# Performance work log

Measured on AMD Instinct MI355X. Metric: run time of the kernel, lower is better.

## Reference

```python
import jax, jax.numpy as jnp
import numpy as np

BS, NUM_RELS, NUM_NODES, EMB = 8, 16, 512, 256


def setup_inputs() -> dict:
    key = jax.random.key(0)
    k1, k2, k3, k4 = jax.random.split(key, 4)
    features = jax.random.normal(k1, (BS, NUM_NODES, EMB), dtype=jnp.float32)
    adjacency = jax.random.uniform(k2, (BS, NUM_RELS, NUM_NODES, NUM_NODES), dtype=jnp.float32)
    # xavier_uniform bounds
    bound = float(np.sqrt(6.0 / (EMB + EMB)))
    W_r = jax.random.uniform(k3, (NUM_RELS, EMB, EMB), minval=-bound, maxval=bound, dtype=jnp.float32)
    W_0 = jax.random.uniform(k4, (EMB, EMB), minval=-bound, maxval=bound, dtype=jnp.float32)
    return {"features": features, "adjacency": adjacency, "W_r": W_r, "W_0": W_0}


def reference(features, adjacency, W_r, W_0):
    # msg[b,r,n,d] = sum_m adjacency[b,r,n,m] * features[b,m,d]
    msg = jnp.einsum('brnm,bmd->brnd', adjacency, features)
    # per-relation projection then sum over relations: [b,n,h]
    features_1 = jnp.einsum('brnd,rdh->bnh', msg, W_r)
    features_2 = jnp.einsum('bnd,dh->bnh', features, W_0)
    return jax.nn.relu(features_1 + features_2)
```

## Files before the change

kernel.cpp:

```cpp
#include <hip/hip_runtime.h>
#include <hip/hip_bf16.h>

#define BS   8
#define NREL 16
#define NN   512
#define EMB  256

typedef float f32x4 __attribute__((ext_vector_type(4)));
typedef short s16x8 __attribute__((ext_vector_type(8)));

__device__ __forceinline__ unsigned short f2bf_bits(float f) {
    union { float f; unsigned u; } v; v.f = f;
    unsigned r = (v.u + 0x7FFFu + ((v.u >> 16) & 1u)) >> 16;
    return (unsigned short)r;
}

__device__ __forceinline__ float bf2f(unsigned short u) {
    union { unsigned u; float f; } v; v.u = ((unsigned)u) << 16;
    return v.f;
}

__device__ __forceinline__ unsigned short f2bf_hw(float f) {
    union { __hip_bfloat16 h; unsigned short u; } v;
    v.h = __float2bfloat16(f);
    return v.u;
}

__global__ __launch_bounds__(256) void k0_prep(
        const float* __restrict__ Wr, const float* __restrict__ W0,
        const float* __restrict__ F,
        unsigned short* __restrict__ wT, unsigned short* __restrict__ Fbf) {
    int bid = blockIdx.x;
    if (bid < 1088) {
        __shared__ float tile[32][33];
        int rel = bid / 64;
        int t   = bid % 64;
        int d0  = (t & 7) * 32;
        int h0  = (t >> 3) * 32;
        int tx  = threadIdx.x & 31;
        int ty  = threadIdx.x >> 5;
        const float* src = (rel < NREL) ? (Wr + rel * (EMB * EMB)) : W0;
#pragma unroll
        for (int k = 0; k < 4; ++k) {
            int d = d0 + ty + k * 8;
            tile[ty + k * 8][tx] = src[d * EMB + h0 + tx];
        }
        __syncthreads();
#pragma unroll
        for (int k = 0; k < 4; ++k) {
            int h = h0 + ty + k * 8;
            wT[(rel * EMB + h) * EMB + d0 + tx] = f2bf_bits(tile[tx][ty + k * 8]);
        }
    } else {
        long i = ((long)(bid - 1088) * 256 + threadIdx.x) * 8;
        f32x4 x0 = *(const f32x4*)(F + i);
        f32x4 x1 = *(const f32x4*)(F + i + 4);
        s16x8 v;
        v[0] = (short)f2bf_bits(x0[0]); v[1] = (short)f2bf_bits(x0[1]);
        v[2] = (short)f2bf_bits(x0[2]); v[3] = (short)f2bf_bits(x0[3]);
        v[4] = (short)f2bf_bits(x1[0]); v[5] = (short)f2bf_bits(x1[1]);
        v[6] = (short)f2bf_bits(x1[2]); v[7] = (short)f2bf_bits(x1[3]);
        *(s16x8*)(Fbf + i) = v;
    }
}

__global__ __launch_bounds__(256) void k1_fw(
        const unsigned short* __restrict__ Fbf, const unsigned short* __restrict__ wT,
        unsigned short* __restrict__ FW, unsigned short* __restrict__ F2b) {
    int bid = blockIdx.x;
    int b   = bid & 7;
    int q   = bid >> 3;
    int rel = q % 17;
    int mt  = q / 17;
    int tid = threadIdx.x;
    int w   = tid >> 6;
    int l   = tid & 63;
    int lg  = l >> 4;
    int lr  = l & 15;

    int h0 = w * 64;
    int m0 = mt * 64;

    const unsigned short* wt = wT + rel * (EMB * EMB) + lg * 8;
    const unsigned short* Fb = Fbf + (long)b * (NN * EMB) + lg * 8;

    f32x4 acc[4][4];
#pragma unroll
    for (int i = 0; i < 4; ++i)
#pragma unroll
        for (int j = 0; j < 4; ++j) acc[i][j] = (f32x4){0.f, 0.f, 0.f, 0.f};

    s16x8 afr[2][4], bfr[2][4];
#pragma unroll
    for (int hi = 0; hi < 4; ++hi)
        afr[0][hi] = *(const s16x8*)(wt + (h0 + hi * 16 + lr) * EMB);
#pragma unroll
    for (int bi = 0; bi < 4; ++bi)
        bfr[0][bi] = *(const s16x8*)(Fb + (m0 + bi * 16 + lr) * EMB);

#pragma unroll
    for (int kk = 0; kk < 8; ++kk) {
        int cur = kk & 1, nxt = cur ^ 1;
        if (kk < 7) {
            int ko = (kk + 1) * 32;
#pragma unroll
            for (int hi = 0; hi < 4; ++hi)
                afr[nxt][hi] = *(const s16x8*)(wt + (h0 + hi * 16 + lr) * EMB + ko);
#pragma unroll
            for (int bi = 0; bi < 4; ++bi)
                bfr[nxt][bi] = *(const s16x8*)(Fb + (m0 + bi * 16 + lr) * EMB + ko);
        }
#pragma unroll
        for (int hi = 0; hi < 4; ++hi)
#pragma unroll
            for (int bi = 0; bi < 4; ++bi)
                acc[hi][bi] = __builtin_amdgcn_mfma_f32_16x16x32_bf16(
                    afr[cur][hi], bfr[cur][bi], acc[hi][bi], 0, 0, 0);
    }

#pragma unroll
    for (int hi = 0; hi < 4; ++hi) {
#pragma unroll
        for (int bi = 0; bi < 4; ++bi) {
            int m  = m0 + bi * 16 + lr;
            int kg = m >> 3, ko = m & 7;
#pragma unroll
            for (int j = 0; j < 4; ++j) {
                int h = h0 + hi * 16 + lg * 4 + j;
                if (rel < NREL)
                    FW[(long)((b * 16 + rel) * 64 + kg) * 2048 + h * 8 + ko] =
                        f2bf_bits(acc[hi][bi][j]);
                else
                    F2b[((long)b * NN + m) * EMB + h] = f2bf_bits(acc[hi][bi][j]);
            }
        }
    }
}

__global__ __launch_bounds__(512, 2) void k2_main(
        const float* __restrict__ adj, const unsigned short* __restrict__ FW,
        unsigned short* __restrict__ part) {
    __shared__ unsigned short Blds[2][16384];
    int bid = blockIdx.x;
    int b   = bid & 7;
    int t   = bid >> 3;
    int nt  = t & 3;
    int rg  = t >> 2;
    int tid = threadIdx.x;
    int w   = tid >> 6;
    int l   = tid & 63;
    int lg  = l >> 4, lr = l & 15;
    int wr  = w >> 1;
    int wc  = w & 1;

    int nrow = nt * 128 + wr * 32;

    f32x4 acc0[16], acc1[16];
#pragma unroll
    for (int i = 0; i < 16; ++i) {
        acc0[i] = (f32x4){0.f, 0.f, 0.f, 0.f};
        acc1[i] = (f32x4){0.f, 0.f, 0.f, 0.f};
    }

    const float* adjb0 =
        adj + (((long)(b * 16 + rg * 2)) * NN + nrow + lr) * NN + lg * 8;
    const float* adjb1 = adjb0 + 16 * NN;
    const unsigned short* fwb = FW + (long)(b * 16 + rg * 2) * 131072;

    s16x8 fwr[4];
    f32x4 ax[2][2], ay[2][2];

#define POFF(p) ((long)((p) >> 3) * 131072 + ((p) & 7) * 16384)

    {
        const unsigned short* s = fwb + POFF(0) + tid * 8;
#pragma unroll
        for (int c = 0; c < 4; ++c) fwr[c] = *(const s16x8*)(s + c * 4096);
#pragma unroll
        for (int c = 0; c < 4; ++c)
            *(s16x8*)(&Blds[0][c * 4096 + tid * 8]) = fwr[c];
    }
    {
        const float* p0 = adjb0 + wc * 32;
        const float* p1 = adjb1 + wc * 32;
        ax[0][0] = *(const f32x4*)p0; ay[0][0] = *(const f32x4*)(p0 + 4);
        ax[0][1] = *(const f32x4*)p1; ay[0][1] = *(const f32x4*)(p1 + 4);
    }
    {
        const unsigned short* s = fwb + POFF(1) + tid * 8;
#pragma unroll
        for (int c = 0; c < 4; ++c) fwr[c] = *(const s16x8*)(s + c * 4096);
    }
    asm volatile("s_waitcnt lgkmcnt(0)" ::: "memory");
    __builtin_amdgcn_sched_barrier(0);
    __builtin_amdgcn_s_barrier();
    asm volatile("" ::: "memory");

#pragma unroll
    for (int i = 0; i < 16; ++i) {
        if (i + 1 < 16) {
            int sl = 2 * (i + 1) + wc;
            long ao = (long)(sl >> 4) * (NN * NN) + (sl & 15) * 32;
            const float* p0 = adjb0 + ao;
            const float* p1 = adjb1 + ao;
            if (((i + 1) & 1) == 0) {
                ax[0][0] = *(const f32x4*)p0; ay[0][0] = *(const f32x4*)(p0 + 4);
                ax[0][1] = *(const f32x4*)p1; ay[0][1] = *(const f32x4*)(p1 + 4);
            } else {
                ax[1][0] = *(const f32x4*)p0; ay[1][0] = *(const f32x4*)(p0 + 4);
                ax[1][1] = *(const f32x4*)p1; ay[1][1] = *(const f32x4*)(p1 + 4);
            }
        }

        f32x4 x00 = ax[i & 1][0], x01 = ay[i & 1][0];
        f32x4 x10 = ax[i & 1][1], x11 = ay[i & 1][1];
        s16x8 a0, a1;
        a0[0] = (short)f2bf_hw(x00[0]); a0[1] = (short)f2bf_hw(x00[1]);
        a0[2] = (short)f2bf_hw(x00[2]); a0[3] = (short)f2bf_hw(x00[3]);
        a0[4] = (short)f2bf_hw(x01[0]); a0[5] = (short)f2bf_hw(x01[1]);
        a0[6] = (short)f2bf_hw(x01[2]); a0[7] = (short)f2bf_hw(x01[3]);
        a1[0] = (short)f2bf_hw(x10[0]); a1[1] = (short)f2bf_hw(x10[1]);
        a1[2] = (short)f2bf_hw(x10[2]); a1[3] = (short)f2bf_hw(x10[3]);
        a1[4] = (short)f2bf_hw(x11[0]); a1[5] = (short)f2bf_hw(x11[1]);
        a1[6] = (short)f2bf_hw(x11[2]); a1[7] = (short)f2bf_hw(x11[3]);

        const unsigned short* bl = &Blds[i & 1][wc * 8192 + lg * 2048];
#pragma unroll
        for (int f = 0; f < 16; ++f) {
            s16x8 bf = *(const s16x8*)(bl + (f * 16 + lr) * 8);
            acc0[f] = __builtin_amdgcn_mfma_f32_16x16x32_bf16(a0, bf, acc0[f], 0, 0, 0);
            acc1[f] = __builtin_amdgcn_mfma_f32_16x16x32_bf16(a1, bf, acc1[f], 0, 0, 0);
        }
        asm volatile("" ::: "memory");

        if (i + 1 < 16) {
            unsigned short* dst = &Blds[(i + 1) & 1][tid * 8];
#pragma unroll
            for (int c = 0; c < 4; ++c) *(s16x8*)(dst + c * 4096) = fwr[c];
            if (i + 2 < 16) {
                const unsigned short* s = fwb + POFF(i + 2) + tid * 8;
#pragma unroll
                for (int c = 0; c < 4; ++c) fwr[c] = *(const s16x8*)(s + c * 4096);
            }
            asm volatile("s_waitcnt lgkmcnt(0)" ::: "memory");
            __builtin_amdgcn_sched_barrier(0);
            __builtin_amdgcn_s_barrier();
            asm volatile("" ::: "memory");
        }
    }
#undef POFF

    float* lf = (float*)Blds;
    unsigned short* pp = part + ((long)rg * BS + b) * (NN * EMB);
#pragma unroll
    for (int g = 0; g < 2; ++g) {
        __syncthreads();
        if (wc == 1) {
#pragma unroll
            for (int f = 0; f < 16; ++f)
#pragma unroll
                for (int j = 0; j < 4; ++j)
                    lf[wr * 4096 + (f * 4 + j) * 64 + l] =
                        g ? acc1[f][j] : acc0[f][j];
        }
        __syncthreads();
        if (wc == 0) {
#pragma unroll
            for (int f = 0; f < 16; ++f) {
                int h = f * 16 + lr;
#pragma unroll
                for (int j = 0; j < 4; ++j) {
                    int n = nrow + g * 16 + lg * 4 + j;
                    float v = (g ? acc1[f][j] : acc0[f][j]) +
                              lf[wr * 4096 + (f * 4 + j) * 64 + l];
                    pp[(long)n * EMB + h] = f2bf_bits(v);
                }
            }
        }
    }
}

__global__ __launch_bounds__(256) void k3_reduce(
        const unsigned short* __restrict__ part,
        const unsigned short* __restrict__ F2b, float* __restrict__ out) {
    const long PS = (long)BS * NN * EMB;
    long i = ((long)blockIdx.x * 256 + threadIdx.x) * 8;
    float s[8];
    {
        s16x8 v = *(const s16x8*)(F2b + i);
#pragma unroll
        for (int j = 0; j < 8; ++j) s[j] = bf2f((unsigned short)v[j]);
    }
#pragma unroll
    for (int rg = 0; rg < 8; ++rg) {
        s16x8 v = *(const s16x8*)(part + (long)rg * PS + i);
#pragma unroll
        for (int j = 0; j < 8; ++j) s[j] += bf2f((unsigned short)v[j]);
    }
    f32x4 r0, r1;
#pragma unroll
    for (int j = 0; j < 4; ++j) {
        r0[j] = s[j] > 0.f ? s[j] : 0.f;
        r1[j] = s[j + 4] > 0.f ? s[j + 4] : 0.f;
    }
    *(f32x4*)(out + i) = r0;
    *(f32x4*)(out + i + 4) = r1;
}

extern "C" void kernel_launch(void* const* d_in, const int* in_sizes, int n_in,
                              void* d_out, int out_size, void* d_ws, size_t ws_size,
                              hipStream_t stream) {
    const float* F   = (const float*)d_in[0];
    const float* adj = (const float*)d_in[1];
    const float* Wr  = (const float*)d_in[2];
    const float* W0  = (const float*)d_in[3];
    float* out = (float*)d_out;

    unsigned short* wT   = (unsigned short*)d_ws;
    unsigned short* Fbf  = wT + 17 * 256 * 256;
    unsigned short* FW   = Fbf + (long)8 * 512 * 256;
    unsigned short* F2b  = FW + (long)8 * 16 * 64 * 2048;
    unsigned short* part = F2b + (long)8 * 512 * 256;

    k0_prep<<<1600, 256, 0, stream>>>(Wr, W0, F, wT, Fbf);
    k1_fw<<<1088, 256, 0, stream>>>(Fbf, wT, FW, F2b);
    k2_main<<<256, 512, 0, stream>>>(adj, FW, part);
    k3_reduce<<<512, 256, 0, stream>>>(part, F2b, out);
}
```

Baseline: 94.53 us.

## Split k2 per relation with H-split waves to double grid and occupancy

```diff
diff --git a/kernel.cpp b/kernel.cpp
--- a/kernel.cpp
+++ b/kernel.cpp
@@ -137,10 +137,10 @@
     }
 }
 
-__global__ __launch_bounds__(512, 2) void k2_main(
+__global__ __launch_bounds__(512, 4) void k2_main(
         const float* __restrict__ adj, const unsigned short* __restrict__ FW,
         unsigned short* __restrict__ part) {
-    __shared__ unsigned short Blds[2][16384];
+    __shared__ unsigned short Blds[2][8192];
     int bid = blockIdx.x;
     int b   = bid & 7;
     int t   = bid >> 3;
@@ -151,45 +151,38 @@
     int l   = tid & 63;
     int lg  = l >> 4, lr = l & 15;
     int wr  = w >> 1;
-    int wc  = w & 1;
-
-    int nrow = nt * 128 + wr * 32;
-
-    f32x4 acc0[16], acc1[16];
-#pragma unroll
-    for (int i = 0; i < 16; ++i) {
-        acc0[i] = (f32x4){0.f, 0.f, 0.f, 0.f};
-        acc1[i] = (f32x4){0.f, 0.f, 0.f, 0.f};
-    }
+    int hh  = w & 1;
+
+    int nrow0 = nt * 128 + wr * 32;
+    int h0    = hh * 128;
+
+    f32x4 acc[2][8];
+#pragma unroll
+    for (int ar = 0; ar < 2; ++ar)
+#pragma unroll
+        for (int f = 0; f < 8; ++f) acc[ar][f] = (f32x4){0.f, 0.f, 0.f, 0.f};
 
     const float* adjb0 =
-        adj + (((long)(b * 16 + rg * 2)) * NN + nrow + lr) * NN + lg * 8;
+        adj + (((long)(b * 16 + rg)) * NN + nrow0 + lr) * NN + lg * 8;
     const float* adjb1 = adjb0 + 16 * NN;
-    const unsigned short* fwb = FW + (long)(b * 16 + rg * 2) * 131072;
-
-    s16x8 fwr[4];
+    const unsigned short* fwb = FW + (long)(b * 16 + rg) * 131072;
+
+    s16x8 fwr[2];
     f32x4 ax[2][2], ay[2][2];
 
-#define POFF(p) ((long)((p) >> 3) * 131072 + ((p) & 7) * 16384)
-
     {
-        const unsigned short* s = fwb + POFF(0) + tid * 8;
-#pragma unroll
-        for (int c = 0; c < 4; ++c) fwr[c] = *(const s16x8*)(s + c * 4096);
-#pragma unroll
-        for (int c = 0; c < 4; ++c)
-            *(s16x8*)(&Blds[0][c * 4096 + tid * 8]) = fwr[c];
-    }
+        const unsigned short* s = fwb + tid * 16;
+        fwr[0] = *(const s16x8*)(s);
+        fwr[1] = *(const s16x8*)(s + 8);
+        *(s16x8*)(&Blds[0][tid * 16])     = fwr[0];
+        *(s16x8*)(&Blds[0][tid * 16 + 8]) = fwr[1];
+    }
+    ax[0][0] = *(const f32x4*)(adjb0); ay[0][0] = *(const f32x4*)(adjb0 + 4);
+    ax[0][1] = *(const f32x4*)(adjb1); ay[0][1] = *(const f32x4*)(adjb1 + 4);
     {
-        const float* p0 = adjb0 + wc * 32;
-        const float* p1 = adjb1 + wc * 32;
-        ax[0][0] = *(const f32x4*)p0; ay[0][0] = *(const f32x4*)(p0 + 4);
-        ax[0][1] = *(const f32x4*)p1; ay[0][1] = *(const f32x4*)(p1 + 4);
-    }
-    {
-        const unsigned short* s = fwb + POFF(1) + tid * 8;
-#pragma unroll
-        for (int c = 0; c < 4; ++c) fwr[c] = *(const s16x8*)(s + c * 4096);
+        const unsigned short* s = fwb + 8192 + tid * 16;
+        fwr[0] = *(const s16x8*)(s);
+        fwr[1] = *(const s16x8*)(s + 8);
     }
     asm volatile("s_waitcnt lgkmcnt(0)" ::: "memory");
     __builtin_amdgcn_sched_barrier(0);
@@ -197,23 +190,19 @@
     asm volatile("" ::: "memory");
 
 #pragma unroll
-    for (int i = 0; i < 16; ++i) {
-        if (i + 1 < 16) {
-            int sl = 2 * (i + 1) + wc;
-            long ao = (long)(sl >> 4) * (NN * NN) + (sl & 15) * 32;
+    for (int s = 0; s < 16; ++s) {
+        if (s + 1 < 16) {
+            long ao = (s + 1) * 32;
             const float* p0 = adjb0 + ao;
             const float* p1 = adjb1 + ao;
-            if (((i + 1) & 1) == 0) {
-                ax[0][0] = *(const f32x4*)p0; ay[0][0] = *(const f32x4*)(p0 + 4);
-                ax[0][1] = *(const f32x4*)p1; ay[0][1] = *(const f32x4*)(p1 + 4);
-            } else {
-                ax[1][0] = *(const f32x4*)p0; ay[1][0] = *(const f32x4*)(p0 + 4);
-                ax[1][1] = *(const f32x4*)p1; ay[1][1] = *(const f32x4*)(p1 + 4);
-            }
-        }
-
-        f32x4 x00 = ax[i & 1][0], x01 = ay[i & 1][0];
-        f32x4 x10 = ax[i & 1][1], x11 = ay[i & 1][1];
+            ax[(s + 1) & 1][0] = *(const f32x4*)p0;
+            ay[(s + 1) & 1][0] = *(const f32x4*)(p0 + 4);
+            ax[(s + 1) & 1][1] = *(const f32x4*)p1;
+            ay[(s + 1) & 1][1] = *(const f32x4*)(p1 + 4);
+        }
+
+        f32x4 x00 = ax[s & 1][0], x01 = ay[s & 1][0];
+        f32x4 x10 = ax[s & 1][1], x11 = ay[s & 1][1];
         s16x8 a0, a1;
         a0[0] = (short)f2bf_hw(x00[0]); a0[1] = (short)f2bf_hw(x00[1]);
         a0[2] = (short)f2bf_hw(x00[2]); a0[3] = (short)f2bf_hw(x00[3]);
@@ -224,23 +213,23 @@
         a1[4] = (short)f2bf_hw(x11[0]); a1[5] = (short)f2bf_hw(x11[1]);
         a1[6] = (short)f2bf_hw(x11[2]); a1[7] = (short)f2bf_hw(x11[3]);
 
-        const unsigned short* bl = &Blds[i & 1][wc * 8192 + lg * 2048];
-#pragma unroll
-        for (int f = 0; f < 16; ++f) {
-            s16x8 bf = *(const s16x8*)(bl + (f * 16 + lr) * 8);
-            acc0[f] = __builtin_amdgcn_mfma_f32_16x16x32_bf16(a0, bf, acc0[f], 0, 0, 0);
-            acc1[f] = __builtin_amdgcn_mfma_f32_16x16x32_bf16(a1, bf, acc1[f], 0, 0, 0);
+        const unsigned short* bl = &Blds[s & 1][lg * 2048 + hh * 1024];
+#pragma unroll
+        for (int f = 0; f < 8; ++f) {
+            s16x8 bf = *(const s16x8*)(bl + f * 128 + lr * 8);
+            acc[0][f] = __builtin_amdgcn_mfma_f32_16x16x32_bf16(a0, bf, acc[0][f], 0, 0, 0);
+            acc[1][f] = __builtin_amdgcn_mfma_f32_16x16x32_bf16(a1, bf, acc[1][f], 0, 0, 0);
         }
         asm volatile("" ::: "memory");
 
-        if (i + 1 < 16) {
-            unsigned short* dst = &Blds[(i + 1) & 1][tid * 8];
-#pragma unroll
-            for (int c = 0; c < 4; ++c) *(s16x8*)(dst + c * 4096) = fwr[c];
-            if (i + 2 < 16) {
-                const unsigned short* s = fwb + POFF(i + 2) + tid * 8;
-#pragma unroll
-                for (int c = 0; c < 4; ++c) fwr[c] = *(const s16x8*)(s + c * 4096);
+        if (s + 1 < 16) {
+            unsigned short* dst = &Blds[(s + 1) & 1][tid * 16];
+            *(s16x8*)(dst)     = fwr[0];
+            *(s16x8*)(dst + 8) = fwr[1];
+            if (s + 2 < 16) {
+                const unsigned short* sp = fwb + (long)(s + 2) * 8192 + tid * 16;
+                fwr[0] = *(const s16x8*)(sp);
+                fwr[1] = *(const s16x8*)(sp + 8);
             }
             asm volatile("s_waitcnt lgkmcnt(0)" ::: "memory");
             __builtin_amdgcn_sched_barrier(0);
@@ -248,33 +237,17 @@
             asm volatile("" ::: "memory");
         }
     }
-#undef POFF
-
-    float* lf = (float*)Blds;
+
     unsigned short* pp = part + ((long)rg * BS + b) * (NN * EMB);
 #pragma unroll
-    for (int g = 0; g < 2; ++g) {
-        __syncthreads();
-        if (wc == 1) {
-#pragma unroll
-            for (int f = 0; f < 16; ++f)
-#pragma unroll
-                for (int j = 0; j < 4; ++j)
-                    lf[wr * 4096 + (f * 4 + j) * 64 + l] =
-                        g ? acc1[f][j] : acc0[f][j];
-        }
-        __syncthreads();
-        if (wc == 0) {
-#pragma unroll
-            for (int f = 0; f < 16; ++f) {
-                int h = f * 16 + lr;
-#pragma unroll
-                for (int j = 0; j < 4; ++j) {
-                    int n = nrow + g * 16 + lg * 4 + j;
-                    float v = (g ? acc1[f][j] : acc0[f][j]) +
-                              lf[wr * 4096 + (f * 4 + j) * 64 + l];
-                    pp[(long)n * EMB + h] = f2bf_bits(v);
-                }
+    for (int ar = 0; ar < 2; ++ar) {
+#pragma unroll
+        for (int f = 0; f < 8; ++f) {
+            int h = h0 + f * 16 + lr;
+#pragma unroll
+            for (int j = 0; j < 4; ++j) {
+                int n = nrow0 + ar * 16 + lg * 4 + j;
+                pp[(long)n * EMB + h] = f2bf_bits(acc[ar][f][j]);
             }
         }
     }
@@ -292,7 +265,7 @@
         for (int j = 0; j < 8; ++j) s[j] = bf2f((unsigned short)v[j]);
     }
 #pragma unroll
-    for (int rg = 0; rg < 8; ++rg) {
+    for (int rg = 0; rg < 16; ++rg) {
         s16x8 v = *(const s16x8*)(part + (long)rg * PS + i);
 #pragma unroll
         for (int j = 0; j < 8; ++j) s[j] += bf2f((unsigned short)v[j]);
@@ -324,6 +297,6 @@
 
     k0_prep<<<1600, 256, 0, stream>>>(Wr, W0, F, wT, Fbf);
     k1_fw<<<1088, 256, 0, stream>>>(Fbf, wT, FW, F2b);
-    k2_main<<<256, 512, 0, stream>>>(adj, FW, part);
+    k2_main<<<512, 512, 0, stream>>>(adj, FW, part);
     k3_reduce<<<512, 256, 0, stream>>>(part, F2b, out);
 }
```

New measurement: 107.5 us. 13.7% more time.

## Stage adjacency tiles through swizzled LDS instead of per-lane global loads

Applied to the files above, without the earlier changes.

```diff
diff --git a/kernel.cpp b/kernel.cpp
--- a/kernel.cpp
+++ b/kernel.cpp
@@ -7,6 +7,7 @@
 #define EMB  256
 
 typedef float f32x4 __attribute__((ext_vector_type(4)));
+typedef short s16x4 __attribute__((ext_vector_type(4)));
 typedef short s16x8 __attribute__((ext_vector_type(8)));
 
 __device__ __forceinline__ unsigned short f2bf_bits(float f) {
@@ -141,6 +142,7 @@
         const float* __restrict__ adj, const unsigned short* __restrict__ FW,
         unsigned short* __restrict__ part) {
     __shared__ unsigned short Blds[2][16384];
+    __shared__ unsigned short AL[2][8192];
     int bid = blockIdx.x;
     int b   = bid & 7;
     int t   = bid >> 3;
@@ -162,15 +164,32 @@
         acc1[i] = (f32x4){0.f, 0.f, 0.f, 0.f};
     }
 
-    const float* adjb0 =
-        adj + (((long)(b * 16 + rg * 2)) * NN + nrow + lr) * NN + lg * 8;
-    const float* adjb1 = adjb0 + 16 * NN;
     const unsigned short* fwb = FW + (long)(b * 16 + rg * 2) * 131072;
+    int pos = tid & 15;
+    int r0s = (tid >> 4) * 4;
+    const float* adjstage =
+        adj + (((long)(b * 16 + rg * 2)) * NN + nt * 128 + r0s) * NN + pos * 4;
 
     s16x8 fwr[4];
-    f32x4 ax[2][2], ay[2][2];
+    f32x4 axr[4];
 
 #define POFF(p) ((long)((p) >> 3) * 131072 + ((p) & 7) * 16384)
+#define ASRC(p) (adjstage + (long)((p) >> 3) * (NN * NN) + ((p) & 7) * 64)
+
+#define ASTAGE(bufidx)                                                        \
+    {                                                                         \
+        _Pragma("unroll")                                                     \
+        for (int g = 0; g < 4; ++g) {                                         \
+            s16x4 v;                                                          \
+            v[0] = (short)f2bf_hw(axr[g][0]);                                 \
+            v[1] = (short)f2bf_hw(axr[g][1]);                                 \
+            v[2] = (short)f2bf_hw(axr[g][2]);                                 \
+            v[3] = (short)f2bf_hw(axr[g][3]);                                 \
+            int rl = r0s + g;                                                 \
+            *(s16x4*)((char*)&AL[bufidx][0] + rl * 128 +                      \
+                      ((pos * 8) ^ ((rl & 7) << 4))) = v;                     \
+        }                                                                     \
+    }
 
     {
         const unsigned short* s = fwb + POFF(0) + tid * 8;
@@ -181,15 +200,18 @@
             *(s16x8*)(&Blds[0][c * 4096 + tid * 8]) = fwr[c];
     }
     {
-        const float* p0 = adjb0 + wc * 32;
-        const float* p1 = adjb1 + wc * 32;
-        ax[0][0] = *(const f32x4*)p0; ay[0][0] = *(const f32x4*)(p0 + 4);
-        ax[0][1] = *(const f32x4*)p1; ay[0][1] = *(const f32x4*)(p1 + 4);
+        const float* s = ASRC(0);
+#pragma unroll
+        for (int g = 0; g < 4; ++g) axr[g] = *(const f32x4*)(s + g * NN);
+        ASTAGE(0);
     }
     {
         const unsigned short* s = fwb + POFF(1) + tid * 8;
 #pragma unroll
         for (int c = 0; c < 4; ++c) fwr[c] = *(const s16x8*)(s + c * 4096);
+        const float* a = ASRC(1);
+#pragma unroll
+        for (int g = 0; g < 4; ++g) axr[g] = *(const f32x4*)(a + g * NN);
     }
     asm volatile("s_waitcnt lgkmcnt(0)" ::: "memory");
     __builtin_amdgcn_sched_barrier(0);
@@ -198,32 +220,15 @@
 
 #pragma unroll
     for (int i = 0; i < 16; ++i) {
-        if (i + 1 < 16) {
-            int sl = 2 * (i + 1) + wc;
-            long ao = (long)(sl >> 4) * (NN * NN) + (sl & 15) * 32;
-            const float* p0 = adjb0 + ao;
-            const float* p1 = adjb1 + ao;
-            if (((i + 1) & 1) == 0) {
-                ax[0][0] = *(const f32x4*)p0; ay[0][0] = *(const f32x4*)(p0 + 4);
-                ax[0][1] = *(const f32x4*)p1; ay[0][1] = *(const f32x4*)(p1 + 4);
-            } else {
-                ax[1][0] = *(const f32x4*)p0; ay[1][0] = *(const f32x4*)(p0 + 4);
-                ax[1][1] = *(const f32x4*)p1; ay[1][1] = *(const f32x4*)(p1 + 4);
-            }
-        }
-
-        f32x4 x00 = ax[i & 1][0], x01 = ay[i & 1][0];
-        f32x4 x10 = ax[i & 1][1], x11 = ay[i & 1][1];
         s16x8 a0, a1;
-        a0[0] = (short)f2bf_hw(x00[0]); a0[1] = (short)f2bf_hw(x00[1]);
-        a0[2] = (short)f2bf_hw(x00[2]); a0[3] = (short)f2bf_hw(x00[3]);
-        a0[4] = (short)f2bf_hw(x01[0]); a0[5] = (short)f2bf_hw(x01[1]);
-        a0[6] = (short)f2bf_hw(x01[2]); a0[7] = (short)f2bf_hw(x01[3]);
-        a1[0] = (short)f2bf_hw(x10[0]); a1[1] = (short)f2bf_hw(x10[1]);
-        a1[2] = (short)f2bf_hw(x10[2]); a1[3] = (short)f2bf_hw(x10[3]);
-        a1[4] = (short)f2bf_hw(x11[0]); a1[5] = (short)f2bf_hw(x11[1]);
-        a1[6] = (short)f2bf_hw(x11[2]); a1[7] = (short)f2bf_hw(x11[3]);
-
+        {
+            int rl0 = wr * 32 + lr;
+            int rl1 = rl0 + 16;
+            a0 = *(const s16x8*)((const char*)&AL[i & 1][0] + rl0 * 128 +
+                                 ((wc * 64 + lg * 16) ^ ((rl0 & 7) << 4)));
+            a1 = *(const s16x8*)((const char*)&AL[i & 1][0] + rl1 * 128 +
+                                 ((wc * 64 + lg * 16) ^ ((rl1 & 7) << 4)));
+        }
         const unsigned short* bl = &Blds[i & 1][wc * 8192 + lg * 2048];
 #pragma unroll
         for (int f = 0; f < 16; ++f) {
@@ -237,10 +242,14 @@
             unsigned short* dst = &Blds[(i + 1) & 1][tid * 8];
 #pragma unroll
             for (int c = 0; c < 4; ++c) *(s16x8*)(dst + c * 4096) = fwr[c];
+            ASTAGE((i + 1) & 1);
             if (i + 2 < 16) {
                 const unsigned short* s = fwb + POFF(i + 2) + tid * 8;
 #pragma unroll
                 for (int c = 0; c < 4; ++c) fwr[c] = *(const s16x8*)(s + c * 4096);
+                const float* a = ASRC(i + 2);
+#pragma unroll
+                for (int g = 0; g < 4; ++g) axr[g] = *(const f32x4*)(a + g * NN);
             }
             asm volatile("s_waitcnt lgkmcnt(0)" ::: "memory");
             __builtin_amdgcn_sched_barrier(0);
@@ -249,6 +258,8 @@
         }
     }
 #undef POFF
+#undef ASRC
+#undef ASTAGE
 
     float* lf = (float*)Blds;
     unsigned short* pp = part + ((long)rg * BS + b) * (NN * EMB);
```

After: 94.99 us. No clear change (+0.5%).

## Halve k2 row tile to double grid and cut accumulator registers

Applied to the files above, without the earlier changes.

```diff
diff --git a/kernel.cpp b/kernel.cpp
--- a/kernel.cpp
+++ b/kernel.cpp
@@ -137,15 +137,15 @@
     }
 }
 
-__global__ __launch_bounds__(512, 2) void k2_main(
+__global__ __launch_bounds__(512, 4) void k2_main(
         const float* __restrict__ adj, const unsigned short* __restrict__ FW,
         unsigned short* __restrict__ part) {
     __shared__ unsigned short Blds[2][16384];
     int bid = blockIdx.x;
     int b   = bid & 7;
     int t   = bid >> 3;
-    int nt  = t & 3;
-    int rg  = t >> 2;
+    int nt  = t & 7;
+    int rg  = t >> 3;
     int tid = threadIdx.x;
     int w   = tid >> 6;
     int l   = tid & 63;
@@ -153,22 +153,18 @@
     int wr  = w >> 1;
     int wc  = w & 1;
 
-    int nrow = nt * 128 + wr * 32;
-
-    f32x4 acc0[16], acc1[16];
-#pragma unroll
-    for (int i = 0; i < 16; ++i) {
-        acc0[i] = (f32x4){0.f, 0.f, 0.f, 0.f};
-        acc1[i] = (f32x4){0.f, 0.f, 0.f, 0.f};
-    }
-
-    const float* adjb0 =
+    int nrow = nt * 64 + wr * 16;
+
+    f32x4 acc[16];
+#pragma unroll
+    for (int i = 0; i < 16; ++i) acc[i] = (f32x4){0.f, 0.f, 0.f, 0.f};
+
+    const float* adjb =
         adj + (((long)(b * 16 + rg * 2)) * NN + nrow + lr) * NN + lg * 8;
-    const float* adjb1 = adjb0 + 16 * NN;
     const unsigned short* fwb = FW + (long)(b * 16 + rg * 2) * 131072;
 
     s16x8 fwr[4];
-    f32x4 ax[2][2], ay[2][2];
+    f32x4 ax[2], ay[2];
 
 #define POFF(p) ((long)((p) >> 3) * 131072 + ((p) & 7) * 16384)
 
@@ -181,10 +177,8 @@
             *(s16x8*)(&Blds[0][c * 4096 + tid * 8]) = fwr[c];
     }
     {
-        const float* p0 = adjb0 + wc * 32;
-        const float* p1 = adjb1 + wc * 32;
-        ax[0][0] = *(const f32x4*)p0; ay[0][0] = *(const f32x4*)(p0 + 4);
-        ax[0][1] = *(const f32x4*)p1; ay[0][1] = *(const f32x4*)(p1 + 4);
+        const float* p0 = adjb + wc * 32;
+        ax[0] = *(const f32x4*)p0; ay[0] = *(const f32x4*)(p0 + 4);
     }
     {
         const unsigned short* s = fwb + POFF(1) + tid * 8;
@@ -201,35 +195,23 @@
         if (i + 1 < 16) {
             int sl = 2 * (i + 1) + wc;
             long ao = (long)(sl >> 4) * (NN * NN) + (sl & 15) * 32;
-            const float* p0 = adjb0 + ao;
-            const float* p1 = adjb1 + ao;
-            if (((i + 1) & 1) == 0) {
-                ax[0][0] = *(const f32x4*)p0; ay[0][0] = *(const f32x4*)(p0 + 4);
-                ax[0][1] = *(const f32x4*)p1; ay[0][1] = *(const f32x4*)(p1 + 4);
-            } else {
-                ax[1][0] = *(const f32x4*)p0; ay[1][0] = *(const f32x4*)(p0 + 4);
-                ax[1][1] = *(const f32x4*)p1; ay[1][1] = *(const f32x4*)(p1 + 4);
-            }
-        }
-
-        f32x4 x00 = ax[i & 1][0], x01 = ay[i & 1][0];
-        f32x4 x10 = ax[i & 1][1], x11 = ay[i & 1][1];
-        s16x8 a0, a1;
-        a0[0] = (short)f2bf_hw(x00[0]); a0[1] = (short)f2bf_hw(x00[1]);
-        a0[2] = (short)f2bf_hw(x00[2]); a0[3] = (short)f2bf_hw(x00[3]);
-        a0[4] = (short)f2bf_hw(x01[0]); a0[5] = (short)f2bf_hw(x01[1]);
-        a0[6] = (short)f2bf_hw(x01[2]); a0[7] = (short)f2bf_hw(x01[3]);
-        a1[0] = (short)f2bf_hw(x10[0]); a1[1] = (short)f2bf_hw(x10[1]);
-        a1[2] = (short)f2bf_hw(x10[2]); a1[3] = (short)f2bf_hw(x10[3]);
-        a1[4] = (short)f2bf_hw(x11[0]); a1[5] = (short)f2bf_hw(x11[1]);
-        a1[6] = (short)f2bf_hw(x11[2]); a1[7] = (short)f2bf_hw(x11[3]);
+            const float* p0 = adjb + ao;
+            ax[(i + 1) & 1] = *(const f32x4*)p0;
+            ay[(i + 1) & 1] = *(const f32x4*)(p0 + 4);
+        }
+
+        f32x4 x0 = ax[i & 1], x1 = ay[i & 1];
+        s16x8 a;
+        a[0] = (short)f2bf_hw(x0[0]); a[1] = (short)f2bf_hw(x0[1]);
+        a[2] = (short)f2bf_hw(x0[2]); a[3] = (short)f2bf_hw(x0[3]);
+        a[4] = (short)f2bf_hw(x1[0]); a[5] = (short)f2bf_hw(x1[1]);
+        a[6] = (short)f2bf_hw(x1[2]); a[7] = (short)f2bf_hw(x1[3]);
 
         const unsigned short* bl = &Blds[i & 1][wc * 8192 + lg * 2048];
 #pragma unroll
         for (int f = 0; f < 16; ++f) {
             s16x8 bf = *(const s16x8*)(bl + (f * 16 + lr) * 8);
-            acc0[f] = __builtin_amdgcn_mfma_f32_16x16x32_bf16(a0, bf, acc0[f], 0, 0, 0);
-            acc1[f] = __builtin_amdgcn_mfma_f32_16x16x32_bf16(a1, bf, acc1[f], 0, 0, 0);
+            acc[f] = __builtin_amdgcn_mfma_f32_16x16x32_bf16(a, bf, acc[f], 0, 0, 0);
         }
         asm volatile("" ::: "memory");
 
@@ -252,29 +234,24 @@
 
     float* lf = (float*)Blds;
     unsigned short* pp = part + ((long)rg * BS + b) * (NN * EMB);
-#pragma unroll
-    for (int g = 0; g < 2; ++g) {
-        __syncthreads();
-        if (wc == 1) {
-#pragma unroll
-            for (int f = 0; f < 16; ++f)
-#pragma unroll
-                for (int j = 0; j < 4; ++j)
-                    lf[wr * 4096 + (f * 4 + j) * 64 + l] =
-                        g ? acc1[f][j] : acc0[f][j];
-        }
-        __syncthreads();
-        if (wc == 0) {
-#pragma unroll
-            for (int f = 0; f < 16; ++f) {
-                int h = f * 16 + lr;
-#pragma unroll
-                for (int j = 0; j < 4; ++j) {
-                    int n = nrow + g * 16 + lg * 4 + j;
-                    float v = (g ? acc1[f][j] : acc0[f][j]) +
-                              lf[wr * 4096 + (f * 4 + j) * 64 + l];
-                    pp[(long)n * EMB + h] = f2bf_bits(v);
-                }
+    __syncthreads();
+    if (wc == 1) {
+#pragma unroll
+        for (int f = 0; f < 16; ++f)
+#pragma unroll
+            for (int j = 0; j < 4; ++j)
+                lf[wr * 4096 + (f * 4 + j) * 64 + l] = acc[f][j];
+    }
+    __syncthreads();
+    if (wc == 0) {
+#pragma unroll
+        for (int f = 0; f < 16; ++f) {
+            int h = f * 16 + lr;
+#pragma unroll
+            for (int j = 0; j < 4; ++j) {
+                int n = nrow + lg * 4 + j;
+                float v = acc[f][j] + lf[wr * 4096 + (f * 4 + j) * 64 + l];
+                pp[(long)n * EMB + h] = f2bf_bits(v);
             }
         }
     }
@@ -324,6 +301,6 @@
 
     k0_prep<<<1600, 256, 0, stream>>>(Wr, W0, F, wT, Fbf);
     k1_fw<<<1088, 256, 0, stream>>>(Fbf, wT, FW, F2b);
-    k2_main<<<256, 512, 0, stream>>>(adj, FW, part);
+    k2_main<<<512, 512, 0, stream>>>(adj, FW, part);
     k3_reduce<<<512, 256, 0, stream>>>(part, F2b, out);
 }
```

New measurement: 104.8 us. 1.11x slower.
